# Optimization experiments

Hardware: AMD Instinct MI355X
Metric: run time of the kernel (lower is better)

Reference implementation:

```python
import jax, jax.numpy as jnp
import numpy as np

N_WIRES = 4
NUM_LAYERS = 3


def _apply_1q(state, U, wire):
    # state: [N,2,2,2,2] complex; U: [2,2] (shared) or [N,2,2] (per-circuit)
    s = jnp.moveaxis(state, 1 + wire, -1)
    if U.ndim == 2:
        s = jnp.einsum('ij,...j->...i', U, s)
    else:
        s = jnp.einsum('nij,n...j->n...i', U, s)
    return jnp.moveaxis(s, -1, 1 + wire)


def _apply_cnot(state, c, t):
    s = jnp.moveaxis(state, (1 + c, 1 + t), (-2, -1))
    s = jnp.stack([s[..., 0, :], s[..., 1, ::-1]], axis=-2)
    return jnp.moveaxis(s, (-2, -1), (1 + c, 1 + t))


def _ry_batched(theta):
    # theta: [N] -> [N,2,2] complex
    c = jnp.cos(theta / 2)
    s = jnp.sin(theta / 2)
    return jnp.stack([jnp.stack([c, -s], -1), jnp.stack([s, c], -1)], -2).astype(jnp.complex64)


def _rot(phi, theta, omega):
    # PennyLane Rot(phi, theta, omega) = RZ(omega) @ RY(theta) @ RZ(phi)
    c = jnp.cos(theta / 2)
    s = jnp.sin(theta / 2)
    m00 = jnp.exp(-1j * (phi + omega) / 2) * c
    m01 = -jnp.exp(1j * (phi - omega) / 2) * s
    m10 = jnp.exp(-1j * (phi - omega) / 2) * s
    m11 = jnp.exp(1j * (phi + omega) / 2) * c
    return jnp.stack([jnp.stack([m00, m01]), jnp.stack([m10, m11])]).astype(jnp.complex64)


def _simulate(angles, params):
    # angles: [N,4] RY data-encoding angles; params: [L,4,3]
    N = angles.shape[0]
    state = jnp.zeros((N, 16), jnp.complex64).at[:, 0].set(1.0).reshape((N, 2, 2, 2, 2))
    # data encoding
    for w in range(N_WIRES):
        state = _apply_1q(state, _ry_batched(angles[:, w]), w)
    # StronglyEntanglingLayers
    for l in range(NUM_LAYERS):
        for w in range(N_WIRES):
            U = _rot(params[l, w, 0], params[l, w, 1], params[l, w, 2])
            state = _apply_1q(state, U, w)
        r = l % (N_WIRES - 1) + 1  # imprimitive range
        for w in range(N_WIRES):
            state = _apply_cnot(state, w, (w + r) % N_WIRES)
    probs = jnp.abs(state.reshape(N, 16)) ** 2
    # <Z_w>: sign = +1 if bit w of basis index is 0 else -1 (wire 0 = MSB)
    bits = (jnp.arange(16)[:, None] >> jnp.arange(3, -1, -1)[None, :]) & 1
    signs = (1 - 2 * bits).astype(probs.dtype)  # [16,4]
    return probs @ signs  # [N,4]


def setup_inputs() -> dict:
    key = jax.random.key(0)
    k1, k2, k3 = jax.random.split(key, 3)
    B = 1024
    x = jax.random.uniform(k1, (B, 1, 28, 28), dtype=jnp.float32)
    params = jax.random.normal(k2, (NUM_LAYERS, N_WIRES, 3), dtype=jnp.float32)
    W = jax.random.normal(k3, (10, N_WIRES * 14 * 14), dtype=jnp.float32) * 0.03
    b = jnp.zeros((10,), dtype=jnp.float32)
    return {"x": x, "params": params, "W": W, "b": b}


def reference(x, params, W, b):
    B = x.shape[0]
    # unfold(2,2,2).unfold(3,2,2) -> [B,14,14,2,2] -> [B*196,4]
    patches = x[:, 0].reshape(B, 14, 2, 14, 2).transpose(0, 1, 3, 2, 4).reshape(B * 196, 4)
    q = _simulate(patches, params).reshape(B, 196 * 4)  # [B,784]
    logits = q @ W.T + b
    return jax.nn.log_softmax(logits, axis=-1)
```

## Files before the change

kernel.cpp:

```cpp
#include <hip/hip_runtime.h>
#include <math.h>

#define QB 2

__device__ static const int PAIR_A[10] = {0,0,0,0,1,1,1,2,2,3};
__device__ static const int PAIR_B[10] = {0,1,2,3,1,2,3,2,3,3};

__device__ __forceinline__ float2 pkfma(float2 a, float b, float2 c) {
    return make_float2(fmaf(a.x, b, c.x), fmaf(a.y, b, c.y));
}

__global__ __launch_bounds__(256) void quanv_fused3_kernel(
    const float* __restrict__ x,
    const float* __restrict__ params,
    const float* __restrict__ Wm,
    const float* __restrict__ bv,
    float* __restrict__ out,
    int B)
{
    __shared__ float4 gm4[12][2];
    __shared__ float Ur[16][17];
    __shared__ float Ui[16][17];
    __shared__ float Amat[4][16][16];
    __shared__ float4 C4s[100];
    __shared__ float q_lds[4][QB][196];
    __shared__ float red[QB][10];

    const int tid  = threadIdx.x;
    const int img0 = blockIdx.x * QB;

    const int pidx = (tid < 196) ? tid : 195;
    const int pi = pidx / 14, pj = pidx % 14;
    float2 r0[QB], r1[QB];
#pragma unroll
    for (int m = 0; m < QB; ++m) {
        const int img = min(img0 + m, B - 1);
        const float* xb = x + img * 784 + pi * 56 + pj * 2;
        r0[m] = *(const float2*)(xb);
        r1[m] = *(const float2*)(xb + 28);
    }

    if (tid < 12) {
        const float phi = params[tid * 3 + 0];
        const float th  = params[tid * 3 + 1];
        const float om  = params[tid * 3 + 2];
        const float aa = 0.5f * (phi + om), ab = 0.5f * (phi - om), at = 0.5f * th;
        const float sa = __sinf(aa), ca = __cosf(aa);
        const float sb = __sinf(ab), cb = __cosf(ab);
        const float st = __sinf(at), ct = __cosf(at);
        gm4[tid][0] = make_float4( ct * ca, -ct * sa, -st * cb, -st * sb);
        gm4[tid][1] = make_float4( ct * ca,  ct * sa,  st * cb, -st * sb);
    }
    __syncthreads();

    {
        const int col = tid >> 4, row = tid & 15;
        float sr = (row == col) ? 1.f : 0.f;
        float si = 0.f;
#pragma unroll
        for (int l = 0; l < 3; ++l) {
#pragma unroll
            for (int w = 0; w < 4; ++w) {
                const int g = l * 4 + w;
                const int m = 8 >> w;
                const int bit = (row & m) ? 1 : 0;
                const float4 mm = gm4[g][bit];
                const float pr = __shfl_xor(sr, m, 64);
                const float pi2 = __shfl_xor(si, m, 64);
                const float nsr = mm.x * sr - mm.y * si + mm.z * pr - mm.w * pi2;
                const float nsi = mm.x * si + mm.y * sr + mm.z * pi2 + mm.w * pr;
                sr = nsr; si = nsi;
            }
            const int r = (l % 3) + 1;
#pragma unroll
            for (int w = 0; w < 4; ++w) {
                const int cm = 8 >> w;
                const int tm = 8 >> ((w + r) & 3);
                const float pr = __shfl_xor(sr, tm, 64);
                const float pi2 = __shfl_xor(si, tm, 64);
                const bool take = (row & cm) != 0;
                sr = take ? pr : sr;
                si = take ? pi2 : si;
            }
        }
        Ur[row][col] = sr;
        Ui[row][col] = si;
    }
    __syncthreads();

    {
        const int i = tid >> 4, j = tid & 15;
        float a0 = 0.f, a1 = 0.f, a2 = 0.f, a3 = 0.f;
#pragma unroll
        for (int k = 0; k < 16; ++k) {
            const float pr = Ur[k][i] * Ur[k][j] + Ui[k][i] * Ui[k][j];
            if (k & 8) a0 -= pr; else a0 += pr;
            if (k & 4) a1 -= pr; else a1 += pr;
            if (k & 2) a2 -= pr; else a2 += pr;
            if (k & 1) a3 -= pr; else a3 += pr;
        }
        Amat[0][i][j] = a0; Amat[1][i][j] = a1;
        Amat[2][i][j] = a2; Amat[3][i][j] = a3;
    }
    __syncthreads();

    for (int e = tid; e < 400; e += 256) {
        const int w = e & 3, pq = e >> 2;
        const int P = pq / 10, Q = pq % 10;
        const int a = PAIR_A[P], b = PAIR_B[P];
        const int c = PAIR_A[Q], d = PAIR_B[Q];
        float val;
        if (a == b && c == d)      val = Amat[w][4 * a + c][4 * a + c];
        else if (a == b)           val = 2.f * Amat[w][4 * a + c][4 * a + d];
        else if (c == d)           val = 2.f * Amat[w][4 * a + c][4 * b + c];
        else                       val = 2.f * (Amat[w][4 * a + c][4 * b + d] +
                                                Amat[w][4 * a + d][4 * b + c]);
        ((float*)&C4s[pq])[w] = val;
    }
    __syncthreads();

    if (tid < 196) {
        float T[QB][10], U[QB][10];
#pragma unroll
        for (int m = 0; m < QB; ++m) {
            const float h0 = 0.5f * r0[m].x, h1 = 0.5f * r0[m].y;
            const float h2 = 0.5f * r1[m].x, h3 = 0.5f * r1[m].y;
            const float s0 = __sinf(h0), c0 = __cosf(h0);
            const float s1 = __sinf(h1), c1 = __cosf(h1);
            const float s2 = __sinf(h2), c2 = __cosf(h2);
            const float s3 = __sinf(h3), c3 = __cosf(h3);
            float t[4], u[4];
            t[0] = c0 * c1; t[1] = c0 * s1; t[2] = s0 * c1; t[3] = s0 * s1;
            u[0] = c2 * c3; u[1] = c2 * s3; u[2] = s2 * c3; u[3] = s2 * s3;
#pragma unroll
            for (int P = 0; P < 10; ++P) {
                T[m][P] = t[PAIR_A[P]] * t[PAIR_B[P]];
                U[m][P] = u[PAIR_A[P]] * u[PAIR_B[P]];
            }
        }

        float2 q01[QB], q23[QB];
#pragma unroll
        for (int m = 0; m < QB; ++m) { q01[m] = make_float2(0.f, 0.f); q23[m] = make_float2(0.f, 0.f); }

#pragma unroll
        for (int P = 0; P < 10; ++P) {
            float2 s01[QB], s23[QB];
#pragma unroll
            for (int m = 0; m < QB; ++m) { s01[m] = make_float2(0.f, 0.f); s23[m] = make_float2(0.f, 0.f); }
#pragma unroll
            for (int Q = 0; Q < 10; ++Q) {
                const float4 cc = C4s[P * 10 + Q];
                const float2 c01 = make_float2(cc.x, cc.y);
                const float2 c23 = make_float2(cc.z, cc.w);
#pragma unroll
                for (int m = 0; m < QB; ++m) {
                    const float uq = U[m][Q];
                    s01[m] = pkfma(c01, uq, s01[m]);
                    s23[m] = pkfma(c23, uq, s23[m]);
                }
            }
#pragma unroll
            for (int m = 0; m < QB; ++m) {
                const float tp = T[m][P];
                q01[m] = pkfma(s01[m], tp, q01[m]);
                q23[m] = pkfma(s23[m], tp, q23[m]);
            }
        }

#pragma unroll
        for (int m = 0; m < QB; ++m) {
            q_lds[0][m][tid] = q01[m].x;
            q_lds[1][m][tid] = q01[m].y;
            q_lds[2][m][tid] = q23[m].x;
            q_lds[3][m][tid] = q23[m].y;
        }
    }
    __syncthreads();

    if (tid < 160) {
        const int img = tid / 80, rem = tid % 80;
        const int o = rem >> 3, c = rem & 7;
        const float4* Wp = (const float4*)Wm;
        float acc = 0.f;
#pragma unroll
        for (int k = 0; k < 25; ++k) {
            const int p = c + 8 * k;
            if (p < 196) {
                const float4 wv = Wp[o * 196 + p];
                acc = fmaf(wv.x, q_lds[0][img][p],
                      fmaf(wv.y, q_lds[1][img][p],
                      fmaf(wv.z, q_lds[2][img][p],
                      fmaf(wv.w, q_lds[3][img][p], acc))));
            }
        }
        acc += __shfl_down(acc, 1, 64);
        acc += __shfl_down(acc, 2, 64);
        acc += __shfl_down(acc, 4, 64);
        if (c == 0) red[img][o] = acc + bv[o];
    }
    __syncthreads();

    if (tid < QB) {
        const int img = img0 + tid;
        if (img < B) {
            float lo[10];
            float mx = -1e30f;
#pragma unroll
            for (int o = 0; o < 10; ++o) { lo[o] = red[tid][o]; mx = fmaxf(mx, lo[o]); }
            float se = 0.f;
#pragma unroll
            for (int o = 0; o < 10; ++o) se += __expf(lo[o] - mx);
            const float lse = mx + __logf(se);
#pragma unroll
            for (int o = 0; o < 10; ++o) out[img * 10 + o] = lo[o] - lse;
        }
    }
}

extern "C" void kernel_launch(void* const* d_in, const int* in_sizes, int n_in,
                              void* d_out, int out_size, void* d_ws, size_t ws_size,
                              hipStream_t stream) {
    const float* x      = (const float*)d_in[0];
    const float* params = (const float*)d_in[1];
    const float* Wm     = (const float*)d_in[2];
    const float* bv     = (const float*)d_in[3];
    float* out          = (float*)d_out;

    const int B = in_sizes[0] / 784;
    const int nblk = (B + QB - 1) / QB;
    quanv_fused3_kernel<<<nblk, 256, 0, stream>>>(x, params, Wm, bv, out, B);
}
```

Baseline: 13.69 us.

## Spread two images across 512 threads, one patch per thread

The block grows from 256 to 512 threads. Each thread now handles one patch of one image, where before each thread looped over two images. The C-coefficient build becomes a single pass over 400 threads using pair tables in shared memory and a branchless scale. The linear layer uses 16 lanes per output with a 4-step shuffle reduction. The intent is to shorten each thread's serial work and cut register pressure. The cost is more idle threads in the unitary stages, which run on only 256 threads, and fewer blocks resident per CU.

```diff
diff --git a/kernel.cpp b/kernel.cpp
--- a/kernel.cpp
+++ b/kernel.cpp
@@ -1,16 +1,14 @@
 #include <hip/hip_runtime.h>
 #include <math.h>
 
-#define QB 2
-
-__device__ static const int PAIR_A[10] = {0,0,0,0,1,1,1,2,2,3};
-__device__ static const int PAIR_B[10] = {0,1,2,3,1,2,3,2,3,3};
+#define IPB 2
+#define BLK 512
 
 __device__ __forceinline__ float2 pkfma(float2 a, float b, float2 c) {
     return make_float2(fmaf(a.x, b, c.x), fmaf(a.y, b, c.y));
 }
 
-__global__ __launch_bounds__(256) void quanv_fused3_kernel(
+__global__ __launch_bounds__(BLK) void quanv_fused4_kernel(
     const float* __restrict__ x,
     const float* __restrict__ params,
     const float* __restrict__ Wm,
@@ -23,21 +21,23 @@
     __shared__ float Ui[16][17];
     __shared__ float Amat[4][16][16];
     __shared__ float4 C4s[100];
-    __shared__ float q_lds[4][QB][196];
-    __shared__ float red[QB][10];
+    __shared__ int   pa_s[10], pb_s[10];
+    __shared__ float q_lds[4][IPB][196];
+    __shared__ float red[IPB][10];
 
     const int tid  = threadIdx.x;
-    const int img0 = blockIdx.x * QB;
-
-    const int pidx = (tid < 196) ? tid : 195;
+    const int img0 = blockIdx.x * IPB;
+
+    const int iml  = (tid >= 196) ? 1 : 0;
+    const int p_raw = tid - iml * 196;
+    const int pidx = (tid < 392) ? p_raw : 0;
     const int pi = pidx / 14, pj = pidx % 14;
-    float2 r0[QB], r1[QB];
-#pragma unroll
-    for (int m = 0; m < QB; ++m) {
-        const int img = min(img0 + m, B - 1);
+    float2 r0, r1;
+    {
+        const int img = min(img0 + iml, B - 1);
         const float* xb = x + img * 784 + pi * 56 + pj * 2;
-        r0[m] = *(const float2*)(xb);
-        r1[m] = *(const float2*)(xb + 28);
+        r0 = *(const float2*)(xb);
+        r1 = *(const float2*)(xb + 28);
     }
 
     if (tid < 12) {
@@ -50,10 +50,15 @@
         const float st = __sinf(at), ct = __cosf(at);
         gm4[tid][0] = make_float4( ct * ca, -ct * sa, -st * cb, -st * sb);
         gm4[tid][1] = make_float4( ct * ca,  ct * sa,  st * cb, -st * sb);
-    }
-    __syncthreads();
-
-    {
+    } else if (tid >= 64 && tid < 74) {
+        const int P = tid - 64;
+        const int pa = (P < 4) ? 0 : (P < 7) ? 1 : (P < 9) ? 2 : 3;
+        const int pb = (P < 4) ? P : (P < 7) ? P - 3 : (P < 9) ? P - 5 : 3;
+        pa_s[P] = pa; pb_s[P] = pb;
+    }
+    __syncthreads();
+
+    if (tid < 256) {
         const int col = tid >> 4, row = tid & 15;
         float sr = (row == col) ? 1.f : 0.f;
         float si = 0.f;
@@ -65,7 +70,7 @@
                 const int m = 8 >> w;
                 const int bit = (row & m) ? 1 : 0;
                 const float4 mm = gm4[g][bit];
-                const float pr = __shfl_xor(sr, m, 64);
+                const float pr  = __shfl_xor(sr, m, 64);
                 const float pi2 = __shfl_xor(si, m, 64);
                 const float nsr = mm.x * sr - mm.y * si + mm.z * pr - mm.w * pi2;
                 const float nsi = mm.x * si + mm.y * sr + mm.z * pi2 + mm.w * pr;
@@ -76,7 +81,7 @@
             for (int w = 0; w < 4; ++w) {
                 const int cm = 8 >> w;
                 const int tm = 8 >> ((w + r) & 3);
-                const float pr = __shfl_xor(sr, tm, 64);
+                const float pr  = __shfl_xor(sr, tm, 64);
                 const float pi2 = __shfl_xor(si, tm, 64);
                 const bool take = (row & cm) != 0;
                 sr = take ? pr : sr;
@@ -88,7 +93,7 @@
     }
     __syncthreads();
 
-    {
+    if (tid < 256) {
         const int i = tid >> 4, j = tid & 15;
         float a0 = 0.f, a1 = 0.f, a2 = 0.f, a3 = 0.f;
 #pragma unroll
@@ -104,88 +109,71 @@
     }
     __syncthreads();
 
-    for (int e = tid; e < 400; e += 256) {
-        const int w = e & 3, pq = e >> 2;
+    if (tid < 400) {
+        const int w = tid & 3, pq = tid >> 2;
         const int P = pq / 10, Q = pq % 10;
-        const int a = PAIR_A[P], b = PAIR_B[P];
-        const int c = PAIR_A[Q], d = PAIR_B[Q];
-        float val;
-        if (a == b && c == d)      val = Amat[w][4 * a + c][4 * a + c];
-        else if (a == b)           val = 2.f * Amat[w][4 * a + c][4 * a + d];
-        else if (c == d)           val = 2.f * Amat[w][4 * a + c][4 * b + c];
-        else                       val = 2.f * (Amat[w][4 * a + c][4 * b + d] +
-                                                Amat[w][4 * a + d][4 * b + c]);
+        const int a = pa_s[P], b = pb_s[P];
+        const int c = pa_s[Q], d = pb_s[Q];
+        const float s = 0.5f * (float)(1 << ((a != b) + (c != d)));
+        const float val = s * (Amat[w][4 * a + c][4 * b + d] +
+                               Amat[w][4 * a + d][4 * b + c]);
         ((float*)&C4s[pq])[w] = val;
     }
     __syncthreads();
 
-    if (tid < 196) {
-        float T[QB][10], U[QB][10];
-#pragma unroll
-        for (int m = 0; m < QB; ++m) {
-            const float h0 = 0.5f * r0[m].x, h1 = 0.5f * r0[m].y;
-            const float h2 = 0.5f * r1[m].x, h3 = 0.5f * r1[m].y;
-            const float s0 = __sinf(h0), c0 = __cosf(h0);
-            const float s1 = __sinf(h1), c1 = __cosf(h1);
-            const float s2 = __sinf(h2), c2 = __cosf(h2);
-            const float s3 = __sinf(h3), c3 = __cosf(h3);
-            float t[4], u[4];
-            t[0] = c0 * c1; t[1] = c0 * s1; t[2] = s0 * c1; t[3] = s0 * s1;
-            u[0] = c2 * c3; u[1] = c2 * s3; u[2] = s2 * c3; u[3] = s2 * s3;
-#pragma unroll
-            for (int P = 0; P < 10; ++P) {
-                T[m][P] = t[PAIR_A[P]] * t[PAIR_B[P]];
-                U[m][P] = u[PAIR_A[P]] * u[PAIR_B[P]];
-            }
-        }
-
-        float2 q01[QB], q23[QB];
-#pragma unroll
-        for (int m = 0; m < QB; ++m) { q01[m] = make_float2(0.f, 0.f); q23[m] = make_float2(0.f, 0.f); }
-
+    if (tid < 392) {
+        const float h0 = 0.5f * r0.x, h1 = 0.5f * r0.y;
+        const float h2 = 0.5f * r1.x, h3 = 0.5f * r1.y;
+        const float s0 = __sinf(h0), c0 = __cosf(h0);
+        const float s1 = __sinf(h1), c1 = __cosf(h1);
+        const float s2 = __sinf(h2), c2 = __cosf(h2);
+        const float s3 = __sinf(h3), c3 = __cosf(h3);
+        float t[4], u[4];
+        t[0] = c0 * c1; t[1] = c0 * s1; t[2] = s0 * c1; t[3] = s0 * s1;
+        u[0] = c2 * c3; u[1] = c2 * s3; u[2] = s2 * c3; u[3] = s2 * s3;
+
+        float T[10], U[10];
+        {
+            int P = 0;
+#pragma unroll
+            for (int a = 0; a < 4; ++a)
+#pragma unroll
+                for (int b2 = a; b2 < 4; ++b2) {
+                    T[P] = t[a] * t[b2];
+                    U[P] = u[a] * u[b2];
+                    ++P;
+                }
+        }
+
+        float2 q01 = make_float2(0.f, 0.f), q23 = make_float2(0.f, 0.f);
 #pragma unroll
         for (int P = 0; P < 10; ++P) {
-            float2 s01[QB], s23[QB];
-#pragma unroll
-            for (int m = 0; m < QB; ++m) { s01[m] = make_float2(0.f, 0.f); s23[m] = make_float2(0.f, 0.f); }
+            float2 s01 = make_float2(0.f, 0.f), s23 = make_float2(0.f, 0.f);
 #pragma unroll
             for (int Q = 0; Q < 10; ++Q) {
                 const float4 cc = C4s[P * 10 + Q];
-                const float2 c01 = make_float2(cc.x, cc.y);
-                const float2 c23 = make_float2(cc.z, cc.w);
-#pragma unroll
-                for (int m = 0; m < QB; ++m) {
-                    const float uq = U[m][Q];
-                    s01[m] = pkfma(c01, uq, s01[m]);
-                    s23[m] = pkfma(c23, uq, s23[m]);
-                }
-            }
-#pragma unroll
-            for (int m = 0; m < QB; ++m) {
-                const float tp = T[m][P];
-                q01[m] = pkfma(s01[m], tp, q01[m]);
-                q23[m] = pkfma(s23[m], tp, q23[m]);
-            }
-        }
-
-#pragma unroll
-        for (int m = 0; m < QB; ++m) {
-            q_lds[0][m][tid] = q01[m].x;
-            q_lds[1][m][tid] = q01[m].y;
-            q_lds[2][m][tid] = q23[m].x;
-            q_lds[3][m][tid] = q23[m].y;
-        }
-    }
-    __syncthreads();
-
-    if (tid < 160) {
-        const int img = tid / 80, rem = tid % 80;
-        const int o = rem >> 3, c = rem & 7;
+                s01 = pkfma(make_float2(cc.x, cc.y), U[Q], s01);
+                s23 = pkfma(make_float2(cc.z, cc.w), U[Q], s23);
+            }
+            q01 = pkfma(s01, T[P], q01);
+            q23 = pkfma(s23, T[P], q23);
+        }
+
+        q_lds[0][iml][p_raw] = q01.x;
+        q_lds[1][iml][p_raw] = q01.y;
+        q_lds[2][iml][p_raw] = q23.x;
+        q_lds[3][iml][p_raw] = q23.y;
+    }
+    __syncthreads();
+
+    if (tid < 320) {
+        const int img = tid / 160, rem = tid % 160;
+        const int o = rem >> 4, c = rem & 15;
         const float4* Wp = (const float4*)Wm;
         float acc = 0.f;
 #pragma unroll
-        for (int k = 0; k < 25; ++k) {
-            const int p = c + 8 * k;
+        for (int k = 0; k < 13; ++k) {
+            const int p = c + 16 * k;
             if (p < 196) {
                 const float4 wv = Wp[o * 196 + p];
                 acc = fmaf(wv.x, q_lds[0][img][p],
@@ -194,14 +182,15 @@
                       fmaf(wv.w, q_lds[3][img][p], acc))));
             }
         }
-        acc += __shfl_down(acc, 1, 64);
-        acc += __shfl_down(acc, 2, 64);
-        acc += __shfl_down(acc, 4, 64);
+        acc += __shfl_down(acc, 1, 16);
+        acc += __shfl_down(acc, 2, 16);
+        acc += __shfl_down(acc, 4, 16);
+        acc += __shfl_down(acc, 8, 16);
         if (c == 0) red[img][o] = acc + bv[o];
     }
     __syncthreads();
 
-    if (tid < QB) {
+    if (tid < IPB) {
         const int img = img0 + tid;
         if (img < B) {
             float lo[10];
@@ -228,6 +217,6 @@
     float* out          = (float*)d_out;
 
     const int B = in_sizes[0] / 784;
-    const int nblk = (B + QB - 1) / QB;
-    quanv_fused3_kernel<<<nblk, 256, 0, stream>>>(x, params, Wm, bv, out, B);
+    const int nblk = (B + IPB - 1) / IPB;
+    quanv_fused4_kernel<<<nblk, BLK, 0, stream>>>(x, params, Wm, bv, out, B);
 }
```

Result: faster. 13.18 us (-3.7%).
